# Performance work log

Hardware: AMD Instinct MI355X
Metric: run time of the kernel (lower is better)

Reference implementation:

```python
import jax, jax.numpy as jnp
import numpy as np

NBATCH, NUP, NDOWN, NMO, NCONF = 8192, 8, 8, 32, 64


def setup_inputs() -> dict:
    key = jax.random.key(0)
    k1, k2, k3, k4 = jax.random.split(key, 4)
    MO = jax.random.normal(k1, (NBATCH, NUP + NDOWN, NMO), dtype=jnp.float32)
    d2MO = jax.random.normal(k2, (NBATCH, NUP + NDOWN, NMO), dtype=jnp.float32)
    # each config = 8 distinct MO column indices per spin (distinct -> invertible A)
    configs_up = jnp.argsort(jax.random.uniform(k3, (NCONF, NMO)), axis=1)[:, :NUP].astype(jnp.int32)
    configs_down = jnp.argsort(jax.random.uniform(k4, (NCONF, NMO)), axis=1)[:, :NDOWN].astype(jnp.int32)
    return {"MO": MO, "d2MO": d2MO, "configs_up": configs_up, "configs_down": configs_down}


def _gather(M, elec_idx, cols):
    # M: (B, nelec, nmo) -> select electron rows then per-config MO columns
    Ms = M[:, elec_idx, :]                  # (B, n, nmo)
    A = jnp.take(Ms, cols, axis=2)          # (B, n, C, n)
    return jnp.transpose(A, (0, 2, 1, 3))   # (B, C, n, n)


def reference(MO, d2MO, configs_up, configs_down):
    nup = configs_up.shape[1]
    ndown = configs_down.shape[1]
    iup = jnp.arange(nup)
    idown = jnp.arange(nup, nup + ndown)

    Aup = _gather(MO, iup, configs_up)       # (B, C, nup, nup)
    Adn = _gather(MO, idown, configs_down)   # (B, C, ndown, ndown)
    d2up = _gather(d2MO, iup, configs_up)
    d2dn = _gather(d2MO, idown, configs_down)

    iAup = jnp.linalg.inv(Aup)
    iAdn = jnp.linalg.inv(Adn)

    # btrace(iA @ d2A) = sum_ij iA[i,j] * d2A[j,i]
    tr = lambda X, Y: jnp.einsum('bcij,bcji->bc', X, Y)
    out = tr(iAup, d2up) + tr(iAdn, d2dn)    # (B, C)

    # return_local_energy=False branch: multiply by product of determinants
    pd = jnp.linalg.det(Aup) * jnp.linalg.det(Adn)
    return -0.5 * out * pd
```

## Files before the change

kernel.cpp:

```cpp
#include <hip/hip_runtime.h>

#define NBATCH 8192
#define NELEC  16
#define NMO    32
#define NCONF  64
#define NS     8
#define TSTR   20
#define TSZ    (NMO * TSTR)
#define TSTRH  24
#define TSZH   (NMO * TSTRH)

typedef float    v2f   __attribute__((ext_vector_type(2)));
typedef _Float16 half8 __attribute__((ext_vector_type(8)));

__device__ __forceinline__ v2f pkfma(v2f a, v2f b, v2f c) {
#if __has_builtin(__builtin_elementwise_fma)
    return __builtin_elementwise_fma(a, b, c);
#else
    return a * b + c;
#endif
}
__device__ __forceinline__ v2f bc2(float s) { return (v2f){s, s}; }
__device__ __forceinline__ float getel2(const v2f (&R)[4], int j) {
    return (j & 1) ? R[j >> 1].y : R[j >> 1].x;
}
__device__ __forceinline__ void setel2(v2f (&R)[4], int j, float v) {
    if (j & 1) R[j >> 1].y = v; else R[j >> 1].x = v;
}

__device__ __forceinline__ void solve8T(const float* __restrict__ MOT,
                                        const _Float16* __restrict__ D2T,
                                        const int (&cols)[NS], int eoff,
                                        float& det_out, float& tr_out)
{
    v2f A2[NS][4];
    #pragma unroll
    for (int j = 0; j < NS; ++j) {
        const float4* pa = (const float4*)(MOT + cols[j] * TSTR + eoff);
        float4 a0 = pa[0], a1 = pa[1];
        A2[j][0] = (v2f){a0.x, a0.y};
        A2[j][1] = (v2f){a0.z, a0.w};
        A2[j][2] = (v2f){a1.x, a1.y};
        A2[j][3] = (v2f){a1.z, a1.w};
    }

    float det = 1.0f;
    #pragma unroll
    for (int k = 0; k < NS; ++k) {
        float ukk = getel2(A2[k], k);
        det *= ukk;
        float pinv = __builtin_amdgcn_rcpf(ukk);
        #pragma unroll
        for (int r = k + 1; r < NS; ++r) {
            float m = getel2(A2[r], k) * pinv;
            v2f m2 = bc2(m);
            #pragma unroll
            for (int p = (k + 1) >> 1; p < 4; ++p)
                A2[r][p] = pkfma(-m2, A2[k][p], A2[r][p]);
            setel2(A2[r], k, m);
        }
        setel2(A2[k], k, pinv);
    }

    float tr = 0.0f;
    #pragma unroll
    for (int t = 0; t < 4; ++t) {
        const int k0 = 2 * t, k1 = 2 * t + 1;

        half8 hd0 = *(const half8*)(D2T + cols[k0] * TSTRH + eoff);
        half8 hd1 = *(const half8*)(D2T + cols[k1] * TSTRH + eoff);

        v2f y2[NS];
        y2[k0] = (v2f){1.0f, 0.0f};
        y2[k1] = (v2f){-getel2(A2[k1], k0), 1.0f};
        #pragma unroll
        for (int i = k1 + 1; i < NS; ++i) {
            v2f acc = (v2f){0.0f, 0.0f};
            #pragma unroll
            for (int j = k0; j < i; ++j)
                acc = pkfma(bc2(getel2(A2[i], j)), y2[j], acc);
            y2[i] = -acc;
        }

        v2f x2[NS];
        #pragma unroll
        for (int i = NS - 1; i >= 0; --i) {
            v2f acc = (i >= k0) ? y2[i] : (v2f){0.0f, 0.0f};
            #pragma unroll
            for (int c2 = i + 1; c2 < NS; ++c2)
                acc = pkfma(-bc2(getel2(A2[i], c2)), x2[c2], acc);
            x2[i] = acc * bc2(getel2(A2[i], i));
        }

        #pragma unroll
        for (int i = 0; i < NS; ++i) {
            tr = fmaf(x2[i].x, (float)hd0[i], tr);
            tr = fmaf(x2[i].y, (float)hd1[i], tr);
        }
    }

    det_out = det;
    tr_out  = tr;
}

__global__ __launch_bounds__(256)
void kp_dh_kernel(const float* __restrict__ MO,
                  const float* __restrict__ d2MO,
                  const int*   __restrict__ cfg_up,
                  const int*   __restrict__ cfg_dn,
                  float*       __restrict__ out)
{
    __shared__ float    smemA[2][TSZ];
    __shared__ _Float16 smemD[2][TSZH];

    const int tid  = threadIdx.x;
    const int half = tid >> 7;
    const int u    = tid & 127;
    const int b    = blockIdx.x * 2 + half;

    float*    MOT = smemA[half];
    _Float16* D2T = smemD[half];

    const float* MOb = MO   + (size_t)b * NELEC * NMO;
    const float* d2b = d2MO + (size_t)b * NELEC * NMO;

    {
        int r = u >> 3;
        int c = (u & 7) * 4;
        float4 v = *(const float4*)(MOb + r * NMO + c);
        float4 w = *(const float4*)(d2b + r * NMO + c);
        MOT[(c + 0) * TSTR + r] = v.x;
        MOT[(c + 1) * TSTR + r] = v.y;
        MOT[(c + 2) * TSTR + r] = v.z;
        MOT[(c + 3) * TSTR + r] = v.w;
        D2T[(c + 0) * TSTRH + r] = (_Float16)w.x;
        D2T[(c + 1) * TSTRH + r] = (_Float16)w.y;
        D2T[(c + 2) * TSTRH + r] = (_Float16)w.z;
        D2T[(c + 3) * TSTRH + r] = (_Float16)w.w;
    }
    __syncthreads();

    const int cidx = u >> 1;
    const int s    = u & 1;
    const int* cfg = s ? cfg_dn : cfg_up;
    int4 c0 = ((const int4*)cfg)[cidx * 2 + 0];
    int4 c1 = ((const int4*)cfg)[cidx * 2 + 1];
    const int cols[NS] = {c0.x, c0.y, c0.z, c0.w, c1.x, c1.y, c1.z, c1.w};

    float det, tr;
    solve8T(MOT, D2T, cols, s * NS, det, tr);

    float det_o = __shfl_xor(det, 1);
    float tr_o  = __shfl_xor(tr, 1);
    if (s == 0)
        out[(size_t)b * NCONF + cidx] = -0.5f * (tr + tr_o) * det * det_o;
}

extern "C" void kernel_launch(void* const* d_in, const int* in_sizes, int n_in,
                              void* d_out, int out_size, void* d_ws, size_t ws_size,
                              hipStream_t stream)
{
    const float* MO     = (const float*)d_in[0];
    const float* d2MO   = (const float*)d_in[1];
    const int*   cfg_up = (const int*)d_in[2];
    const int*   cfg_dn = (const int*)d_in[3];
    float* out = (float*)d_out;

    dim3 grid(NBATCH / 2);
    dim3 block(256);
    kp_dh_kernel<<<grid, block, 0, stream>>>(MO, d2MO, cfg_up, cfg_dn, out);
}
```

Measured before the change: 89.33 us.

## Remap to one wave per batch with each thread solving both spin determinants

New measurement: 92.75 us. +3.8%, slower.

```diff
diff --git a/kernel.cpp b/kernel.cpp
--- a/kernel.cpp
+++ b/kernel.cpp
@@ -103,57 +103,53 @@
     tr_out  = tr;
 }
 
-__global__ __launch_bounds__(256)
-void kp_dh_kernel(const float* __restrict__ MO,
+__global__ __launch_bounds__(64)
+void kp_w1_kernel(const float* __restrict__ MO,
                   const float* __restrict__ d2MO,
                   const int*   __restrict__ cfg_up,
                   const int*   __restrict__ cfg_dn,
                   float*       __restrict__ out)
 {
-    __shared__ float    smemA[2][TSZ];
-    __shared__ _Float16 smemD[2][TSZH];
+    __shared__ float    smA[TSZ];
+    __shared__ _Float16 smD[TSZH];
 
-    const int tid  = threadIdx.x;
-    const int half = tid >> 7;
-    const int u    = tid & 127;
-    const int b    = blockIdx.x * 2 + half;
-
-    float*    MOT = smemA[half];
-    _Float16* D2T = smemD[half];
+    const int w = threadIdx.x;
+    const int b = blockIdx.x;
 
     const float* MOb = MO   + (size_t)b * NELEC * NMO;
     const float* d2b = d2MO + (size_t)b * NELEC * NMO;
 
     {
-        int r = u >> 3;
-        int c = (u & 7) * 4;
-        float4 v = *(const float4*)(MOb + r * NMO + c);
-        float4 w = *(const float4*)(d2b + r * NMO + c);
-        MOT[(c + 0) * TSTR + r] = v.x;
-        MOT[(c + 1) * TSTR + r] = v.y;
-        MOT[(c + 2) * TSTR + r] = v.z;
-        MOT[(c + 3) * TSTR + r] = v.w;
-        D2T[(c + 0) * TSTRH + r] = (_Float16)w.x;
-        D2T[(c + 1) * TSTRH + r] = (_Float16)w.y;
-        D2T[(c + 2) * TSTRH + r] = (_Float16)w.z;
-        D2T[(c + 3) * TSTRH + r] = (_Float16)w.w;
+        const int c = (w & 7) * 4;
+        #pragma unroll
+        for (int rr = 0; rr < 2; ++rr) {
+            const int r = (w >> 3) + rr * 8;
+            float4 v = *(const float4*)(MOb + r * NMO + c);
+            float4 d = *(const float4*)(d2b + r * NMO + c);
+            smA[(c + 0) * TSTR + r] = v.x;
+            smA[(c + 1) * TSTR + r] = v.y;
+            smA[(c + 2) * TSTR + r] = v.z;
+            smA[(c + 3) * TSTR + r] = v.w;
+            smD[(c + 0) * TSTRH + r] = (_Float16)d.x;
+            smD[(c + 1) * TSTRH + r] = (_Float16)d.y;
+            smD[(c + 2) * TSTRH + r] = (_Float16)d.z;
+            smD[(c + 3) * TSTRH + r] = (_Float16)d.w;
+        }
     }
     __syncthreads();
 
-    const int cidx = u >> 1;
-    const int s    = u & 1;
-    const int* cfg = s ? cfg_dn : cfg_up;
-    int4 c0 = ((const int4*)cfg)[cidx * 2 + 0];
-    int4 c1 = ((const int4*)cfg)[cidx * 2 + 1];
-    const int cols[NS] = {c0.x, c0.y, c0.z, c0.w, c1.x, c1.y, c1.z, c1.w};
+    int4 u0 = ((const int4*)cfg_up)[w * 2 + 0];
+    int4 u1 = ((const int4*)cfg_up)[w * 2 + 1];
+    int4 d0 = ((const int4*)cfg_dn)[w * 2 + 0];
+    int4 d1 = ((const int4*)cfg_dn)[w * 2 + 1];
+    const int cu[NS] = {u0.x, u0.y, u0.z, u0.w, u1.x, u1.y, u1.z, u1.w};
+    const int cd[NS] = {d0.x, d0.y, d0.z, d0.w, d1.x, d1.y, d1.z, d1.w};
 
-    float det, tr;
-    solve8T(MOT, D2T, cols, s * NS, det, tr);
+    float detU, trU, detD, trD;
+    solve8T(smA, smD, cu, 0,  detU, trU);
+    solve8T(smA, smD, cd, NS, detD, trD);
 
-    float det_o = __shfl_xor(det, 1);
-    float tr_o  = __shfl_xor(tr, 1);
-    if (s == 0)
-        out[(size_t)b * NCONF + cidx] = -0.5f * (tr + tr_o) * det * det_o;
+    out[(size_t)b * NCONF + w] = -0.5f * (trU + trD) * detU * detD;
 }
 
 extern "C" void kernel_launch(void* const* d_in, const int* in_sizes, int n_in,
@@ -166,7 +162,7 @@
     const int*   cfg_dn = (const int*)d_in[3];
     float* out = (float*)d_out;
 
-    dim3 grid(NBATCH / 2);
-    dim3 block(256);
-    kp_dh_kernel<<<grid, block, 0, stream>>>(MO, d2MO, cfg_up, cfg_dn, out);
+    dim3 grid(NBATCH);
+    dim3 block(64);
+    kp_w1_kernel<<<grid, block, 0, stream>>>(MO, d2MO, cfg_up, cfg_dn, out);
 }
```
